# Kernel optimization log

Measured on AMD Instinct MI355X. Metric: run time of the kernel, lower is better.

## Reference

```python
import jax, jax.numpy as jnp
import numpy as np

N, IN_FEAT, LAT_FEAT, OUT_FEAT = 131072, 128, 128, 256
NUM_EXPERTS, TOP_K, OMEGA = 8, 2, 30.0


def setup_inputs() -> dict:
    key = jax.random.key(0)
    ks = jax.random.split(key, 8)
    u = lambda k_, shape, lim: jax.random.uniform(k_, shape, jnp.float32, -lim, lim)
    w_lim = np.sqrt(6.0 / IN_FEAT) / OMEGA  # SIREN init for non-first layers
    return {
        "x": jax.random.normal(ks[0], (N, IN_FEAT), jnp.float32),
        "latents": jax.random.normal(ks[1], (N, LAT_FEAT), jnp.float32),
        "gate_w": u(ks[2], (IN_FEAT, NUM_EXPERTS), 1.0 / np.sqrt(IN_FEAT)),
        "gate_b": jnp.zeros((NUM_EXPERTS,), jnp.float32),
        "W": u(ks[3], (NUM_EXPERTS, IN_FEAT, OUT_FEAT), w_lim),
        "b": u(ks[4], (NUM_EXPERTS, OUT_FEAT), 1.0 / np.sqrt(IN_FEAT)),
        "Wl": u(ks[5], (NUM_EXPERTS, LAT_FEAT, 2 * OUT_FEAT), 1.0 / np.sqrt(LAT_FEAT)),
        "bl": u(ks[6], (NUM_EXPERTS, 2 * OUT_FEAT), 1.0 / np.sqrt(LAT_FEAT)),
    }


def reference(x, latents, gate_w, gate_b, W, b, Wl, bl):
    # Gating: top-k over expert logits, softmax over the selected k logits.
    logits = x @ gate_w + gate_b                      # [N, E]
    top_vals, top_idx = jax.lax.top_k(logits, TOP_K)  # [N, k]
    top_w = jax.nn.softmax(top_vals, axis=-1)         # [N, k]
    # Dense combine weights: combine[n, e] = sum_i top_w[n, i] * (top_idx[n,i]==e).
    # Mathematically identical to the masked gather/scatter loop in torch.
    combine = jnp.sum(
        jax.nn.one_hot(top_idx, NUM_EXPERTS, dtype=x.dtype) * top_w[..., None],
        axis=1,
    )  # [N, E]
    out = jnp.zeros((x.shape[0], OUT_FEAT), x.dtype)
    for e in range(NUM_EXPERTS):  # fixed small loop over experts
        h = x @ W[e] + b[e]                    # [N, out]
        lat = latents @ Wl[e] + bl[e]          # [N, 2*out]
        scale, shift = lat[:, :OUT_FEAT], lat[:, OUT_FEAT:]
        out = out + combine[:, e:e + 1] * jnp.sin(OMEGA * h * scale + shift)
    return (out, latents)
```

## Files before the change

kernel.cpp:

```cpp
#include <hip/hip_runtime.h>

#define INF_  128
#define OUTF  256
#define LATF  128
#define OUT2  512
#define NEXP  8
#define OMEGA_ 30.0f

typedef float  f32x4  __attribute__((ext_vector_type(4)));
typedef __bf16 bf16x8 __attribute__((ext_vector_type(8)));
typedef unsigned short ushort8 __attribute__((ext_vector_type(8)));

#define PACK_THREADS (NEXP * 4 * 4 * 3 * 4 * 64)
#define EXP_STRIDE   (4 * 4 * 3 * 4 * 512)
#define PH_STRIDE    6144
#define GEMM_GRID    1056

__device__ __forceinline__ unsigned short bfbits(float f) {
    unsigned int u = __builtin_bit_cast(unsigned int, f);
    return (unsigned short)((u + 0x7FFFu + ((u >> 16) & 1u)) >> 16);
}

__device__ __forceinline__ bf16x8 cvt8(f32x4 a, f32x4 b) {
    bf16x8 r;
    r[0] = (__bf16)a.x; r[1] = (__bf16)a.y; r[2] = (__bf16)a.z; r[3] = (__bf16)a.w;
    r[4] = (__bf16)b.x; r[5] = (__bf16)b.y; r[6] = (__bf16)b.z; r[7] = (__bf16)b.w;
    return r;
}

__device__ __forceinline__ f32x4 bload(const unsigned short* p) {
    const ushort4 u = *(const ushort4*)p;
    f32x4 r;
    r.x = __builtin_bit_cast(float, (unsigned int)u.x << 16);
    r.y = __builtin_bit_cast(float, (unsigned int)u.y << 16);
    r.z = __builtin_bit_cast(float, (unsigned int)u.z << 16);
    r.w = __builtin_bit_cast(float, (unsigned int)u.w << 16);
    return r;
}

#define GLOAD_LDS16(g, l) __builtin_amdgcn_global_load_lds( \
    (const __attribute__((address_space(1))) unsigned int*)(g), \
    (__attribute__((address_space(3))) unsigned int*)(l), 16, 0, 0)

__global__ void prep_kernel(const float* __restrict__ x,
                            const float* __restrict__ lat,
                            const float* __restrict__ gw,
                            const float* __restrict__ gb,
                            const float* __restrict__ W,
                            const float* __restrict__ Wl,
                            unsigned short* __restrict__ eidx,
                            float2* __restrict__ wpair,
                            unsigned int* __restrict__ cnt,
                            float* __restrict__ lat_out,
                            unsigned short* __restrict__ Bpk,
                            int nGate)
{
    __shared__ float sgw[INF_ * NEXP];
    __shared__ int lc[64];
    const int tid = threadIdx.x;

    if ((int)blockIdx.x >= nGate) {
        const int t = ((int)blockIdx.x - nGate) * 256 + tid;
        if (t >= PACK_THREADS) return;
        const int l   = t & 63;
        const int ks  = (t >> 6) & 3;
        const int m3  = (t >> 8) % 3;
        const int g   = (t >> 8) / 3;
        const int nf  = g & 3, nc = (g >> 2) & 3, e = g >> 4;
        const int col = nc * 64 + nf * 16 + (l & 15);
        const int kb  = ks * 32 + (l >> 4) * 8;
        ushort8 o;
#pragma unroll
        for (int j = 0; j < 8; ++j) {
            float v;
            if (m3 == 0) v = W [((size_t)e * 128 + kb + j) * 256 + col];
            else         v = Wl[((size_t)e * 128 + kb + j) * 512 + col + (m3 == 2 ? 256 : 0)];
            o[j] = bfbits(v);
        }
        *(ushort8*)(Bpk + (size_t)t * 8) = o;
        return;
    }

    ((float4*)sgw)[tid] = ((const float4*)gw)[tid];
    if (tid < 64) lc[tid] = 0;
    __syncthreads();

    const int t = blockIdx.x * 256 + tid;
    float acc[8];
#pragma unroll
    for (int e = 0; e < 8; ++e) acc[e] = gb[e];
    const float4* xr = (const float4*)(x + (size_t)t * INF_);
#pragma unroll 8
    for (int i = 0; i < 32; ++i) {
        float4 v = xr[i];
#pragma unroll
        for (int j = 0; j < 4; ++j) {
            const float xk = (&v.x)[j];
            const float4 g0 = *(const float4*)&sgw[(i * 4 + j) * 8];
            const float4 g1 = *(const float4*)&sgw[(i * 4 + j) * 8 + 4];
            acc[0] += xk * g0.x; acc[1] += xk * g0.y; acc[2] += xk * g0.z; acc[3] += xk * g0.w;
            acc[4] += xk * g1.x; acc[5] += xk * g1.y; acc[6] += xk * g1.z; acc[7] += xk * g1.w;
        }
    }
    float best = -1e30f, sec = -1e30f; int bi = 0, si = 0;
#pragma unroll
    for (int e = 0; e < 8; ++e) {
        const float v = acc[e];
        if (v > best)      { sec = best; si = bi; best = v; bi = e; }
        else if (v > sec)  { sec = v; si = e; }
    }
    const float ew  = __expf(sec - best);
    const float inv = 1.0f / (1.0f + ew);
    const float wb  = inv, wsc = ew * inv;
    int emin, emax; float wmin, wmax;
    if (bi < si) { emin = bi; wmin = wb;  emax = si; wmax = wsc; }
    else         { emin = si; wmin = wsc; emax = bi; wmax = wb;  }
    const int pid = emin * 8 + emax;
    eidx[t]  = (unsigned short)pid;
    wpair[t] = make_float2(wmin, wmax);
    atomicAdd(&lc[pid], 1);
    __syncthreads();
    if (tid < 64) { if (lc[tid]) atomicAdd(&cnt[tid], (unsigned int)lc[tid]); }

    const f32x4* lr = (const f32x4*)(lat) + (size_t)blockIdx.x * 8192;
    f32x4*       lo = (f32x4*)(lat_out)   + (size_t)blockIdx.x * 8192;
#pragma unroll
    for (int i = 0; i < 32; ++i) {
        f32x4 v = lr[tid + i * 256];
        __builtin_nontemporal_store(v, &lo[tid + i * 256]);
    }
}

__global__ void scan_kernel(unsigned int* __restrict__ c, unsigned int* __restrict__ table)
{
    const int p = threadIdx.x;
    const unsigned int n = c[p];
    unsigned int s = n;
#pragma unroll
    for (int d = 1; d < 64; d <<= 1) {
        unsigned int t = __shfl_up(s, d);
        if (p >= d) s += t;
    }
    const unsigned int excl = s - n;
    c[64 + p] = excl; c[128 + p] = excl;
    const unsigned int nt = (n + 127) >> 7;
    unsigned int ts = nt;
#pragma unroll
    for (int d = 1; d < 64; d <<= 1) {
        unsigned int t = __shfl_up(ts, d);
        if (p >= d) ts += t;
    }
    const unsigned int texcl = ts - nt;
    for (unsigned int t = 0; t < nt; ++t) table[texcl + t] = (unsigned int)p | (t << 6);
    if (p == 63) c[192] = texcl + nt;
}

__global__ void scatter_kernel(const unsigned short* __restrict__ eidx,
                               const float2* __restrict__ wpair,
                               unsigned int* __restrict__ cur,
                               unsigned int* __restrict__ perm,
                               float2* __restrict__ wps)
{
    __shared__ int lc[64];
    __shared__ unsigned int lbase[64];
    const int tid = threadIdx.x;
    if (tid < 64) lc[tid] = 0;
    __syncthreads();
    const int t = blockIdx.x * 256 + tid;
    const int pid = eidx[t];
    const float2 w = wpair[t];
    const int p = atomicAdd(&lc[pid], 1);
    __syncthreads();
    if (tid < 64) { lbase[tid] = lc[tid] ? atomicAdd(&cur[tid], (unsigned int)lc[tid]) : 0u; }
    __syncthreads();
    const unsigned int q = lbase[pid] + (unsigned int)p;
    perm[q] = (unsigned int)t;
    wps[q]  = w;
}

__launch_bounds__(256, 3)
__global__ void moe_gemm_kernel(const float* __restrict__ x,
                                const float* __restrict__ lat,
                                const unsigned short* __restrict__ Bpk,
                                const float* __restrict__ bias,
                                const float* __restrict__ biasl,
                                const unsigned int* __restrict__ c,
                                const unsigned int* __restrict__ table,
                                const unsigned int* __restrict__ perm,
                                const float2* __restrict__ wps,
                                float* __restrict__ out)
{
    __shared__ __align__(16) unsigned short sB[2][2 * PH_STRIDE];
    __shared__ __align__(16) unsigned short sbias[6 * 256];

    const unsigned int ntiles = c[192];
    const unsigned int d = blockIdx.x;
    const unsigned int bid = (d & 7) * (GEMM_GRID / 8) + (d >> 3);
    if (bid >= ntiles) return;
    const unsigned int ent = table[bid];
    const int pid  = ent & 63;
    const int tile = ent >> 6;
    const int emin = pid >> 3, emax = pid & 7;
    const unsigned int cn  = c[pid];
    const unsigned int off = c[64 + pid] + (unsigned int)tile * 128u;
    const int rows = min(128, (int)(cn - (unsigned int)tile * 128u));
    const unsigned int* permS = perm + off;
    const float2* wS = wps + off;

    const int tid  = threadIdx.x;
    const int lane = tid & 63;
    const int w    = tid >> 6;
    const int lrow = lane & 15;
    const int lgrp = lane >> 4;
    const int half = tid >> 7;
    const int wh   = (tid >> 6) & 1;
    const int t7   = tid & 127;

    const int r0 = w * 32 + lrow, r1 = r0 + 16;
    const int t0 = (int)permS[min(r0, rows - 1)];
    const int t1 = (int)permS[min(r1, rows - 1)];
    const float2 w0 = wS[min(r0, rows - 1)];
    const float2 w1 = wS[min(r1, rows - 1)];
    bf16x8 ax[2][4], al[2][4];
    {
        const float* x0 = x   + (size_t)t0 * INF_;
        const float* x1 = x   + (size_t)t1 * INF_;
        const float* l0 = lat + (size_t)t0 * LATF;
        const float* l1 = lat + (size_t)t1 * LATF;
#pragma unroll
        for (int ks = 0; ks < 4; ++ks) {
            const int kb = ks * 32 + lgrp * 8;
            ax[0][ks] = cvt8(__builtin_nontemporal_load((const f32x4*)(x0 + kb)),
                             __builtin_nontemporal_load((const f32x4*)(x0 + kb + 4)));
            ax[1][ks] = cvt8(__builtin_nontemporal_load((const f32x4*)(x1 + kb)),
                             __builtin_nontemporal_load((const f32x4*)(x1 + kb + 4)));
            al[0][ks] = cvt8(__builtin_nontemporal_load((const f32x4*)(l0 + kb)),
                             __builtin_nontemporal_load((const f32x4*)(l0 + kb + 4)));
            al[1][ks] = cvt8(__builtin_nontemporal_load((const f32x4*)(l1 + kb)),
                             __builtin_nontemporal_load((const f32x4*)(l1 + kb + 4)));
        }
    }

    const unsigned short* B0 = Bpk + (size_t)emin * EXP_STRIDE;
    const unsigned short* B1 = Bpk + (size_t)emax * EXP_STRIDE;
    const unsigned short* Bh = half ? B1 : B0;

    {
        const int i4 = (tid & 63) * 4;
        const int sg = tid >> 6;
#pragma unroll
        for (int rep = 0; rep < 2; ++rep) {
            const int seg = sg + rep * 4;
            if (seg < 6) {
                const float* bsrc =
                    (seg == 0) ? bias  + emin * OUTF :
                    (seg == 1) ? bias  + emax * OUTF :
                    (seg == 2) ? biasl + emin * OUT2 :
                    (seg == 3) ? biasl + emin * OUT2 + 256 :
                    (seg == 4) ? biasl + emax * OUT2 :
                                 biasl + emax * OUT2 + 256;
                const f32x4 v = *(const f32x4*)(bsrc + i4);
                ushort4 u;
                u.x = bfbits(v.x); u.y = bfbits(v.y); u.z = bfbits(v.z); u.w = bfbits(v.w);
                *(ushort4*)&sbias[seg * 256 + i4] = u;
            }
        }
    }

    auto STAGE = [&](int ph, int buf) {
        const unsigned short* src = Bh + (size_t)ph * PH_STRIDE + (size_t)t7 * 8;
        unsigned short* dst = &sB[buf][half * PH_STRIDE + wh * 512];
#pragma unroll
        for (int r = 0; r < 6; ++r)
            GLOAD_LDS16(src + r * 1024, dst + r * 1024);
    };

    f32x4 acc[2][3][2];
    auto COMPUTE = [&](int buf) {
#pragma unroll
        for (int ex = 0; ex < 2; ++ex)
#pragma unroll
            for (int m = 0; m < 3; ++m)
#pragma unroll
                for (int mf = 0; mf < 2; ++mf) acc[ex][m][mf] = (f32x4)0.0f;
#pragma unroll
        for (int ex = 0; ex < 2; ++ex) {
#pragma unroll
            for (int m = 0; m < 3; ++m) {
                bf16x8 bb[4];
#pragma unroll
                for (int ks = 0; ks < 4; ++ks)
                    bb[ks] = *(const bf16x8*)&sB[buf][ex * PH_STRIDE + (m * 4 + ks) * 512 + lane * 8];
#pragma unroll
                for (int ks = 0; ks < 4; ++ks) {
#pragma unroll
                    for (int mf = 0; mf < 2; ++mf) {
                        const bf16x8 a = (m == 0) ? ax[mf][ks] : al[mf][ks];
                        acc[ex][m][mf] = __builtin_amdgcn_mfma_f32_16x16x32_bf16(bb[ks], a, acc[ex][m][mf], 0, 0, 0);
                    }
                }
            }
        }
    };

    auto EPILOGUE = [&](int ph, bool guard) {
        const int cb = ph * 16 + lgrp * 4;
        const f32x4 b0h = bload(&sbias[0 * 256 + cb]);
        const f32x4 b1h = bload(&sbias[1 * 256 + cb]);
        const f32x4 b0s = bload(&sbias[2 * 256 + cb]);
        const f32x4 b0f = bload(&sbias[3 * 256 + cb]);
        const f32x4 b1s = bload(&sbias[4 * 256 + cb]);
        const f32x4 b1f = bload(&sbias[5 * 256 + cb]);
#pragma unroll
        for (int mf = 0; mf < 2; ++mf) {
            const int  rr  = mf ? r1 : r0;
            if (guard && rr >= rows) continue;
            const int  tok = mf ? t1 : t0;
            const float wmn = mf ? w1.x : w0.x;
            const float wmx = mf ? w1.y : w0.y;
            f32x4 v;
#pragma unroll
            for (int j = 0; j < 4; ++j) {
                const float h0 = acc[0][0][mf][j] + b0h[j];
                const float s0 = acc[0][1][mf][j] + b0s[j];
                const float f0 = acc[0][2][mf][j] + b0f[j];
                const float h1 = acc[1][0][mf][j] + b1h[j];
                const float s1 = acc[1][1][mf][j] + b1s[j];
                const float f1 = acc[1][2][mf][j] + b1f[j];
                v[j] = wmn * __sinf(OMEGA_ * h0 * s0 + f0)
                     + wmx * __sinf(OMEGA_ * h1 * s1 + f1);
            }
            __builtin_nontemporal_store(v, (f32x4*)(out + (size_t)tok * OUTF + cb));
        }
    };

    STAGE(0, 0);
    asm volatile("s_waitcnt vmcnt(0) lgkmcnt(0)" ::: "memory");
    __builtin_amdgcn_s_barrier();
    __builtin_amdgcn_sched_barrier(0);

    if (rows == 128) {
#pragma unroll 1
        for (int ph = 0; ph < 16; ++ph) {
            const int buf = ph & 1;
            if (ph < 15) STAGE(ph + 1, buf ^ 1);
            COMPUTE(buf);
            EPILOGUE(ph, false);
            __builtin_amdgcn_sched_barrier(0);
            if (ph < 15) {
                asm volatile("s_waitcnt vmcnt(2)" ::: "memory");
                __builtin_amdgcn_s_barrier();
                __builtin_amdgcn_sched_barrier(0);
            }
        }
    } else {
#pragma unroll 1
        for (int ph = 0; ph < 16; ++ph) {
            const int buf = ph & 1;
            if (ph > 0) {
                STAGE(ph, buf);
                asm volatile("s_waitcnt vmcnt(0)" ::: "memory");
                __builtin_amdgcn_s_barrier();
                __builtin_amdgcn_sched_barrier(0);
            }
            COMPUTE(buf);
            EPILOGUE(ph, true);
            __builtin_amdgcn_s_barrier();
            __builtin_amdgcn_sched_barrier(0);
        }
    }
}

extern "C" void kernel_launch(void* const* d_in, const int* in_sizes, int n_in,
                              void* d_out, int out_size, void* d_ws, size_t ws_size,
                              hipStream_t stream)
{
    const float* x   = (const float*)d_in[0];
    const float* lat = (const float*)d_in[1];
    const float* gw  = (const float*)d_in[2];
    const float* gb  = (const float*)d_in[3];
    const float* W   = (const float*)d_in[4];
    const float* b   = (const float*)d_in[5];
    const float* Wl  = (const float*)d_in[6];
    const float* bl  = (const float*)d_in[7];
    float* out = (float*)d_out;
    const int N = in_sizes[0] / INF_;

    char* ws = (char*)d_ws;
    unsigned int*   cnt   = (unsigned int*)ws;
    unsigned int*   table = (unsigned int*)(ws + 1024);
    unsigned short* eidx  = (unsigned short*)(ws + 8192);
    float2*         wpair = (float2*)(ws + 8192 + 2 * (size_t)N);
    unsigned int*   perm  = (unsigned int*)(ws + 8192 + 10 * (size_t)N);
    float2*         wps   = (float2*)(ws + 8192 + 14 * (size_t)N);
    unsigned short* Bpk   = (unsigned short*)(ws + 8192 + 22 * (size_t)N);

    (void)hipMemsetAsync(cnt, 0, 256, stream);

    const int nGate = N / 256;
    prep_kernel<<<dim3(nGate + PACK_THREADS / 256), 256, 0, stream>>>(
        x, lat, gw, gb, W, Wl, eidx, wpair, cnt, out + (size_t)N * OUTF, Bpk, nGate);
    scan_kernel<<<1, 64, 0, stream>>>(cnt, table);
    scatter_kernel<<<dim3(N / 256), 256, 0, stream>>>(eidx, wpair, cnt + 128, perm, wps);

    moe_gemm_kernel<<<dim3(GEMM_GRID), 256, 0, stream>>>(x, lat, Bpk, b, bl,
                                                         cnt, table, perm, wps, out);
}
```

Before: 164.0 us.

## Fuse gate scatter into prep and move latent copy into GEMM kernel

Removes the separate scan and scatter kernels. The prep kernel now writes permutation indices directly into fixed-capacity per-pair buckets (pid*CAP), and each GEMM block rebuilds the tile table with a wave prefix-sum and ballot over the counts. The latent passthrough copy moves from the prep kernel into extra blocks of the GEMM launch so it overlaps with compute. The intent is to cut launch overhead and intermediate eidx/wpair traffic, at the cost of a much larger workspace (64×CAP buckets) and a redundant scan in every GEMM block.

```diff
diff --git a/kernel.cpp b/kernel.cpp
--- a/kernel.cpp
+++ b/kernel.cpp
@@ -14,7 +14,9 @@
 #define PACK_THREADS (NEXP * 4 * 4 * 3 * 4 * 64)
 #define EXP_STRIDE   (4 * 4 * 3 * 4 * 512)
 #define PH_STRIDE    6144
-#define GEMM_GRID    1056
+#define GEMM_COMPUTE 1056
+#define COPY_BLOCKS  512
+#define CAP          131072
 
 __device__ __forceinline__ unsigned short bfbits(float f) {
     unsigned int u = __builtin_bit_cast(unsigned int, f);
@@ -43,20 +45,19 @@
     (__attribute__((address_space(3))) unsigned int*)(l), 16, 0, 0)
 
 __global__ void prep_kernel(const float* __restrict__ x,
-                            const float* __restrict__ lat,
                             const float* __restrict__ gw,
                             const float* __restrict__ gb,
                             const float* __restrict__ W,
                             const float* __restrict__ Wl,
-                            unsigned short* __restrict__ eidx,
-                            float2* __restrict__ wpair,
-                            unsigned int* __restrict__ cnt,
-                            float* __restrict__ lat_out,
+                            unsigned int* __restrict__ cur,
+                            unsigned int* __restrict__ perm,
+                            float2* __restrict__ wps,
                             unsigned short* __restrict__ Bpk,
                             int nGate)
 {
     __shared__ float sgw[INF_ * NEXP];
     __shared__ int lc[64];
+    __shared__ unsigned int lbase[64];
     const int tid = threadIdx.x;
 
     if ((int)blockIdx.x >= nGate) {
@@ -116,66 +117,14 @@
     if (bi < si) { emin = bi; wmin = wb;  emax = si; wmax = wsc; }
     else         { emin = si; wmin = wsc; emax = bi; wmax = wb;  }
     const int pid = emin * 8 + emax;
-    eidx[t]  = (unsigned short)pid;
-    wpair[t] = make_float2(wmin, wmax);
-    atomicAdd(&lc[pid], 1);
-    __syncthreads();
-    if (tid < 64) { if (lc[tid]) atomicAdd(&cnt[tid], (unsigned int)lc[tid]); }
-
-    const f32x4* lr = (const f32x4*)(lat) + (size_t)blockIdx.x * 8192;
-    f32x4*       lo = (f32x4*)(lat_out)   + (size_t)blockIdx.x * 8192;
-#pragma unroll
-    for (int i = 0; i < 32; ++i) {
-        f32x4 v = lr[tid + i * 256];
-        __builtin_nontemporal_store(v, &lo[tid + i * 256]);
-    }
-}
-
-__global__ void scan_kernel(unsigned int* __restrict__ c, unsigned int* __restrict__ table)
-{
-    const int p = threadIdx.x;
-    const unsigned int n = c[p];
-    unsigned int s = n;
-#pragma unroll
-    for (int d = 1; d < 64; d <<= 1) {
-        unsigned int t = __shfl_up(s, d);
-        if (p >= d) s += t;
-    }
-    const unsigned int excl = s - n;
-    c[64 + p] = excl; c[128 + p] = excl;
-    const unsigned int nt = (n + 127) >> 7;
-    unsigned int ts = nt;
-#pragma unroll
-    for (int d = 1; d < 64; d <<= 1) {
-        unsigned int t = __shfl_up(ts, d);
-        if (p >= d) ts += t;
-    }
-    const unsigned int texcl = ts - nt;
-    for (unsigned int t = 0; t < nt; ++t) table[texcl + t] = (unsigned int)p | (t << 6);
-    if (p == 63) c[192] = texcl + nt;
-}
-
-__global__ void scatter_kernel(const unsigned short* __restrict__ eidx,
-                               const float2* __restrict__ wpair,
-                               unsigned int* __restrict__ cur,
-                               unsigned int* __restrict__ perm,
-                               float2* __restrict__ wps)
-{
-    __shared__ int lc[64];
-    __shared__ unsigned int lbase[64];
-    const int tid = threadIdx.x;
-    if (tid < 64) lc[tid] = 0;
-    __syncthreads();
-    const int t = blockIdx.x * 256 + tid;
-    const int pid = eidx[t];
-    const float2 w = wpair[t];
+
     const int p = atomicAdd(&lc[pid], 1);
     __syncthreads();
     if (tid < 64) { lbase[tid] = lc[tid] ? atomicAdd(&cur[tid], (unsigned int)lc[tid]) : 0u; }
     __syncthreads();
-    const unsigned int q = lbase[pid] + (unsigned int)p;
+    const size_t q = (size_t)pid * CAP + lbase[pid] + (unsigned int)p;
     perm[q] = (unsigned int)t;
-    wps[q]  = w;
+    wps[q]  = make_float2(wmin, wmax);
 }
 
 __launch_bounds__(256, 3)
@@ -185,30 +134,52 @@
                                 const float* __restrict__ bias,
                                 const float* __restrict__ biasl,
                                 const unsigned int* __restrict__ c,
-                                const unsigned int* __restrict__ table,
                                 const unsigned int* __restrict__ perm,
                                 const float2* __restrict__ wps,
-                                float* __restrict__ out)
+                                float* __restrict__ out,
+                                float* __restrict__ lat_out)
 {
     __shared__ __align__(16) unsigned short sB[2][2 * PH_STRIDE];
     __shared__ __align__(16) unsigned short sbias[6 * 256];
 
-    const unsigned int ntiles = c[192];
-    const unsigned int d = blockIdx.x;
-    const unsigned int bid = (d & 7) * (GEMM_GRID / 8) + (d >> 3);
+    const unsigned int dd = blockIdx.x;
+    const int tid  = threadIdx.x;
+
+    if (dd >= GEMM_COMPUTE) {
+        const int cb = (int)dd - GEMM_COMPUTE;
+        const f32x4* src = (const f32x4*)lat + (size_t)cb * 8192;
+        f32x4*       dst = (f32x4*)lat_out   + (size_t)cb * 8192;
+#pragma unroll
+        for (int i = 0; i < 32; ++i) {
+            f32x4 v = __builtin_nontemporal_load(&src[tid + i * 256]);
+            __builtin_nontemporal_store(v, &dst[tid + i * 256]);
+        }
+        return;
+    }
+
+    const unsigned int bid = (dd & 7) * (GEMM_COMPUTE / 8) + (dd >> 3);
+    const int lane = tid & 63;
+
+    const unsigned int n_l  = c[lane];
+    const unsigned int nt_l = (n_l + 127) >> 7;
+    unsigned int ts = nt_l;
+#pragma unroll
+    for (int s = 1; s < 64; s <<= 1) {
+        unsigned int tt = __shfl_up(ts, s);
+        if (lane >= s) ts += tt;
+    }
+    const unsigned int texcl  = ts - nt_l;
+    const unsigned int ntiles = __shfl(ts, 63);
     if (bid >= ntiles) return;
-    const unsigned int ent = table[bid];
-    const int pid  = ent & 63;
-    const int tile = ent >> 6;
+    const unsigned long long mk = __ballot(bid >= texcl);
+    const int pid  = __popcll(mk) - 1;
+    const int tile = (int)(bid - __shfl(texcl, pid));
+    const unsigned int cn = __shfl(n_l, pid);
     const int emin = pid >> 3, emax = pid & 7;
-    const unsigned int cn  = c[pid];
-    const unsigned int off = c[64 + pid] + (unsigned int)tile * 128u;
     const int rows = min(128, (int)(cn - (unsigned int)tile * 128u));
-    const unsigned int* permS = perm + off;
-    const float2* wS = wps + off;
-
-    const int tid  = threadIdx.x;
-    const int lane = tid & 63;
+    const unsigned int* permS = perm + (size_t)pid * CAP + (size_t)tile * 128u;
+    const float2* wS = wps + (size_t)pid * CAP + (size_t)tile * 128u;
+
     const int w    = tid >> 6;
     const int lrow = lane & 15;
     const int lgrp = lane >> 4;
@@ -387,22 +358,17 @@
     const int N = in_sizes[0] / INF_;
 
     char* ws = (char*)d_ws;
-    unsigned int*   cnt   = (unsigned int*)ws;
-    unsigned int*   table = (unsigned int*)(ws + 1024);
-    unsigned short* eidx  = (unsigned short*)(ws + 8192);
-    float2*         wpair = (float2*)(ws + 8192 + 2 * (size_t)N);
-    unsigned int*   perm  = (unsigned int*)(ws + 8192 + 10 * (size_t)N);
-    float2*         wps   = (float2*)(ws + 8192 + 14 * (size_t)N);
-    unsigned short* Bpk   = (unsigned short*)(ws + 8192 + 22 * (size_t)N);
-
-    (void)hipMemsetAsync(cnt, 0, 256, stream);
+    unsigned int*   cur  = (unsigned int*)ws;
+    unsigned short* Bpk  = (unsigned short*)(ws + 4096);
+    unsigned int*   perm = (unsigned int*)(ws + (4096 + 2 * (size_t)EXP_STRIDE * NEXP + 4096));
+    float2*         wps  = (float2*)((char*)perm + (size_t)64 * CAP * sizeof(unsigned int));
+
+    (void)hipMemsetAsync(cur, 0, 256, stream);
 
     const int nGate = N / 256;
     prep_kernel<<<dim3(nGate + PACK_THREADS / 256), 256, 0, stream>>>(
-        x, lat, gw, gb, W, Wl, eidx, wpair, cnt, out + (size_t)N * OUTF, Bpk, nGate);
-    scan_kernel<<<1, 64, 0, stream>>>(cnt, table);
-    scatter_kernel<<<dim3(N / 256), 256, 0, stream>>>(eidx, wpair, cnt + 128, perm, wps);
-
-    moe_gemm_kernel<<<dim3(GEMM_GRID), 256, 0, stream>>>(x, lat, Bpk, b, bl,
-                                                         cnt, table, perm, wps, out);
-}
+        x, gw, gb, W, Wl, cur, perm, wps, Bpk, nGate);
+
+    moe_gemm_kernel<<<dim3(GEMM_COMPUTE + COPY_BLOCKS), 256, 0, stream>>>(
+        x, lat, Bpk, b, bl, cur, perm, wps, out, out + (size_t)N * OUTF);
+}
```

Measured after the change: 155.7 us. 5.1% less time.
